# Performance work log

Measured on AMD Instinct MI355X. Metric: run time of the kernel, lower is better.

Reference implementation:

```python
import jax, jax.numpy as jnp
import numpy as np

B, T, C = 4, 4096, 1024
H = 16
D = C // H
EPS = 1e-06


def setup_inputs() -> dict:
    key = jax.random.key(0)
    k1, k2, k3 = jax.random.split(key, 3)
    x = jax.random.normal(k1, (B, T, C), dtype=jnp.float32)
    Wqkv = jax.random.normal(k2, (3 * C, C), dtype=jnp.float32) * (1.0 / np.sqrt(C))
    Wproj = jax.random.normal(k3, (C, C), dtype=jnp.float32) * (1.0 / np.sqrt(C))
    bproj = jnp.zeros((C,), dtype=jnp.float32)
    return {"x": x, "Wqkv": Wqkv, "Wproj": Wproj, "bproj": bproj}


def _phi(x):
    # elu(x) + 1 kernel feature map (non-negative)
    return jax.nn.elu(x) + 1.0


def reference(x, Wqkv, Wproj, bproj):
    b, t, c = x.shape
    qkv = jnp.einsum('btc,ec->bte', x, Wqkv)              # (B,T,3C)
    qkv = qkv.reshape(b, t, 3, H, D)
    q, k, v = qkv[:, :, 0], qkv[:, :, 1], qkv[:, :, 2]     # (B,T,H,D)
    q = _phi(q)
    k = _phi(k)
    # kv state: sum over sequence of outer products k_d v_m -> (B,H,D,D)
    kv = jnp.einsum('bnhd,bnhm->bhdm', k, v)
    k_sum = k.sum(axis=1)                                  # (B,H,D)
    out = jnp.einsum('bnhd,bhdm->bnhm', q, kv)             # (B,T,H,D)
    normalizer = jnp.einsum('bnhd,bhd->bnh', q, k_sum) + EPS
    out = out / normalizer[..., None]
    out = out.reshape(b, t, c)
    out = jnp.einsum('btc,oc->bto', out, Wproj) + bproj
    return out
```

## Files before the change

### kernel.cpp

```cpp
#include <hip/hip_runtime.h>

typedef __bf16 bf16;
typedef bf16 bf16x8 __attribute__((ext_vector_type(8)));
typedef bf16 bf16x4 __attribute__((ext_vector_type(4)));
typedef float f32x4 __attribute__((ext_vector_type(4)));

#define B_ 4
#define T_ 4096
#define C_ 1024
#define EPS_ 1e-6f
#define KVTSTR 16448

typedef __attribute__((address_space(1))) const void* as1p;
typedef __attribute__((address_space(3))) void* as3p;

__global__ void cast_kernel(const float* __restrict__ in, bf16* __restrict__ out, int n8) {
  int i = blockIdx.x * blockDim.x + threadIdx.x;
  int stride = gridDim.x * blockDim.x;
  for (; i < n8; i += stride) {
    const float4* p = (const float4*)(in + (size_t)i * 8);
    float4 v0 = p[0];
    float4 v1 = p[1];
    bf16x8 o;
    o[0] = (bf16)v0.x; o[1] = (bf16)v0.y; o[2] = (bf16)v0.z; o[3] = (bf16)v0.w;
    o[4] = (bf16)v1.x; o[5] = (bf16)v1.y; o[6] = (bf16)v1.z; o[7] = (bf16)v1.w;
    *(bf16x8*)(out + (size_t)i * 8) = o;
  }
}

#define BM 256
#define BN 128
#define BK 32
#define KD 1024
#define NT (KD / BK)
#define ABYT (BM * BK * 2)
#define BUFB ((BM + BN) * BK * 2)
#define SMEMB (6 * BUFB)

#define GSTEP(CURA, CURB, NXTA, NXTB, T)                                                   \
  do {                                                                                     \
    const bool pf = (T) + 5 < NT;                                                          \
    if (pf) {                                                                              \
      const int ko = ((T) + 5) * BK;                                                       \
      __builtin_amdgcn_global_load_lds((as1p)(pA0 + ko), (as3p)(smem + sb + tid * 16), 16, 0, 0);          \
      __builtin_amdgcn_global_load_lds((as1p)(pA1 + ko), (as3p)(smem + sb + 8192 + tid * 16), 16, 0, 0);   \
      __builtin_amdgcn_global_load_lds((as1p)(pB0 + ko), (as3p)(smem + sb + 16384 + tid * 16), 16, 0, 0);  \
    }                                                                                      \
    {                                                                                      \
      const bf16* Ab = (const bf16*)(smem + rb);                                           \
      const bf16* Bb = (const bf16*)(smem + rb + ABYT);                                    \
      _Pragma("unroll") for (int mi = 0; mi < 4; mi++)                                     \
          NXTA[mi] = *(const bf16x8*)(Ab + (wm * 64 + mi * 16 + fr) * 32 + fsw);           \
      _Pragma("unroll") for (int nj = 0; nj < 4; nj++)                                     \
          NXTB[nj] = *(const bf16x8*)(Bb + (wn * 64 + nj * 16 + fr) * 32 + fsw);           \
    }                                                                                      \
    __builtin_amdgcn_s_setprio(1);                                                         \
    _Pragma("unroll") for (int mi = 0; mi < 4; mi++)                                       \
        _Pragma("unroll") for (int nj = 0; nj < 4; nj++)                                   \
            acc[mi][nj] = __builtin_amdgcn_mfma_f32_16x16x32_bf16(CURA[mi], CURB[nj], acc[mi][nj], 0, 0, 0); \
    __builtin_amdgcn_s_setprio(0);                                                         \
    asm volatile("s_waitcnt lgkmcnt(0)" ::: "memory");                                     \
    if (pf) asm volatile("s_waitcnt vmcnt(9)" ::: "memory");                               \
    else    asm volatile("s_waitcnt vmcnt(0)" ::: "memory");                               \
    __builtin_amdgcn_s_barrier();                                                          \
    __builtin_amdgcn_sched_barrier(0);                                                     \
    rb += BUFB; if (rb >= SMEMB) rb -= SMEMB;                                              \
    sb += BUFB; if (sb >= SMEMB) sb -= SMEMB;                                              \
  } while (0)

template <int MODE>
__global__ __launch_bounds__(512, 1) void gemm5(
    const bf16* __restrict__ A, const bf16* __restrict__ Bm,
    void* __restrict__ Cout, const float* __restrict__ bias,
    bf16* __restrict__ kvt, int M, int N, int tiles_n) {
  extern __shared__ char smem[];
  const int tid = threadIdx.x;
  const int l = tid & 63;
  const int w = tid >> 6;
  const int wm = w >> 1;
  const int wn = w & 1;

  const int cpx = gridDim.x >> 3;
  const int bid = (blockIdx.x & 7) * cpx + (blockIdx.x >> 3);
  const int tm = (bid / tiles_n) * BM;
  const int tn = (bid % tiles_n) * BN;

  const int srow = tid >> 2;
  const int g8 = ((tid & 3) ^ ((tid >> 3) & 3)) * 8;

  const bf16* pA0 = A + (size_t)(tm + srow) * KD + g8;
  const bf16* pA1 = A + (size_t)(tm + 128 + srow) * KD + g8;
  const bf16* pB0 = Bm + (size_t)(tn + srow) * KD + g8;

  const int fr = l & 15;
  const int fc = l >> 4;
  const int fsw = (fc ^ ((fr >> 1) & 3)) * 8;

  f32x4 acc[4][4] = {};
  bf16x8 afA[4], bfA[4], afB[4], bfB[4];

#pragma unroll
  for (int kt = 0; kt < 5; kt++) {
    __builtin_amdgcn_global_load_lds((as1p)(pA0 + kt * BK), (as3p)(smem + kt * BUFB + tid * 16), 16, 0, 0);
    __builtin_amdgcn_global_load_lds((as1p)(pA1 + kt * BK), (as3p)(smem + kt * BUFB + 8192 + tid * 16), 16, 0, 0);
    __builtin_amdgcn_global_load_lds((as1p)(pB0 + kt * BK), (as3p)(smem + kt * BUFB + 16384 + tid * 16), 16, 0, 0);
  }
  asm volatile("s_waitcnt vmcnt(9)" ::: "memory");
  __builtin_amdgcn_s_barrier();
  __builtin_amdgcn_sched_barrier(0);

  {
    const bf16* Ab = (const bf16*)(smem);
    const bf16* Bb = (const bf16*)(smem + ABYT);
#pragma unroll
    for (int mi = 0; mi < 4; mi++)
      afA[mi] = *(const bf16x8*)(Ab + (wm * 64 + mi * 16 + fr) * 32 + fsw);
#pragma unroll
    for (int nj = 0; nj < 4; nj++)
      bfA[nj] = *(const bf16x8*)(Bb + (wn * 64 + nj * 16 + fr) * 32 + fsw);
  }

  int rb = BUFB;
  int sb = 5 * BUFB;
  for (int t = 0; t < NT; t += 2) {
    GSTEP(afA, bfA, afB, bfB, t);
    GSTEP(afB, bfB, afA, bfA, t + 1);
  }

  const int crow0 = tm + wm * 64 + (l >> 4) * 4;
  const int ccol0 = tn + wn * 64 + (l & 15);
  if (MODE == 0) {
    if (tn < 1024) {
      bf16* qbuf = (bf16*)Cout;
#pragma unroll
      for (int mi = 0; mi < 4; mi++)
#pragma unroll
        for (int nj = 0; nj < 4; nj++) {
          const int col = ccol0 + nj * 16;
#pragma unroll
          for (int r = 0; r < 4; r++) {
            const int row = crow0 + mi * 16 + r;
            float v = acc[mi][nj][r];
            v = (v > 0.f) ? (v + 1.0f) : __expf(v);
            qbuf[(size_t)row * 1024 + col] = (bf16)v;
          }
        }
    } else {
#pragma unroll
      for (int mi = 0; mi < 4; mi++)
#pragma unroll
        for (int nj = 0; nj < 4; nj++) {
          const int colp = ccol0 + nj * 16 - 1024;
          const bool isk = (colp < 1024);
          bf16x4 pk;
#pragma unroll
          for (int r = 0; r < 4; r++) {
            float v = acc[mi][nj][r];
            if (isk) v = (v > 0.f) ? (v + 1.0f) : __expf(v);
            pk[r] = (bf16)v;
          }
          const int n0 = crow0 + mi * 16;
          *(bf16x4*)(kvt + (size_t)colp * KVTSTR + n0) = pk;
        }
    }
  } else {
    float* Cf = (float*)Cout;
#pragma unroll
    for (int mi = 0; mi < 4; mi++)
#pragma unroll
      for (int nj = 0; nj < 4; nj++) {
        const int col = ccol0 + nj * 16;
        const float bv = bias[col];
#pragma unroll
        for (int r = 0; r < 4; r++) {
          const int row = crow0 + mi * 16 + r;
          Cf[(size_t)row * N + col] = acc[mi][nj][r] + bv;
        }
      }
  }
}

__global__ __launch_bounds__(256) void kvgemm(const bf16* __restrict__ kvt,
                                              float* __restrict__ partial) {
  const int kc = blockIdx.x >> 6;
  const int bh = blockIdx.x & 63;
  const int b = bh >> 4, h = bh & 15;
  const int l = threadIdx.x & 63;
  const int w = threadIdx.x >> 6;

  const size_t nb = (size_t)b * 4096 + kc * 1024 + (l >> 4) * 8;
  const bf16* Ar = kvt + (size_t)(h * 64 + w * 16 + (l & 15)) * KVTSTR + nb;
  const bf16* Br = kvt + (size_t)(1024 + h * 64 + (l & 15)) * KVTSTR + nb;

  f32x4 acc[4] = {};
  float ks = 0.f;
  bf16x8 aC, bC[4], aN, bN[4];
  aC = *(const bf16x8*)Ar;
#pragma unroll
  for (int nj = 0; nj < 4; nj++) bC[nj] = *(const bf16x8*)(Br + (size_t)nj * 16 * KVTSTR);

  for (int it = 0; it < 32; ++it) {
    if (it + 1 < 32) {
      aN = *(const bf16x8*)(Ar + (it + 1) * 32);
#pragma unroll
      for (int nj = 0; nj < 4; nj++)
        bN[nj] = *(const bf16x8*)(Br + (size_t)nj * 16 * KVTSTR + (it + 1) * 32);
    }
#pragma unroll
    for (int i = 0; i < 8; i++) ks += (float)aC[i];
#pragma unroll
    for (int nj = 0; nj < 4; nj++)
      acc[nj] = __builtin_amdgcn_mfma_f32_16x16x32_bf16(aC, bC[nj], acc[nj], 0, 0, 0);
    aC = aN;
#pragma unroll
    for (int nj = 0; nj < 4; nj++) bC[nj] = bN[nj];
  }

  ks += __shfl_xor(ks, 16);
  ks += __shfl_xor(ks, 32);

  float* p = partial + (size_t)(kc * 64 + bh) * 4160;
#pragma unroll
  for (int nj = 0; nj < 4; nj++) {
    const int m = nj * 16 + (l & 15);
#pragma unroll
    for (int r = 0; r < 4; r++) {
      const int d = w * 16 + (l >> 4) * 4 + r;
      p[d * 64 + m] = acc[nj][r];
    }
  }
  if (l < 16) p[4096 + w * 16 + l] = ks;
}

__global__ void kv_finalize(const float* __restrict__ partial, bf16* __restrict__ kvb) {
  const int bh = blockIdx.x;
  for (int i = threadIdx.x; i < 80 * 64; i += 256) {
    const int row = i >> 6;
    const int dd = i & 63;
    float outv = 0.f;
    if (row < 64) {
      float s = 0.f;
#pragma unroll
      for (int kc = 0; kc < 4; kc++)
        s += partial[(size_t)(kc * 64 + bh) * 4160 + dd * 64 + row];
      outv = s;
    } else if (row < 66) {
      float s = 0.f;
#pragma unroll
      for (int kc = 0; kc < 4; kc++)
        s += partial[(size_t)(kc * 64 + bh) * 4160 + 4096 + dd];
      bf16 hi = (bf16)s;
      outv = (row == 64) ? (float)hi : (s - (float)hi);
    }
    kvb[(size_t)bh * 5120 + row * 64 + dd] = (bf16)outv;
  }
}

__global__ __launch_bounds__(256) void attn_mfma(const bf16* __restrict__ qbuf,
                                                 const bf16* __restrict__ kvb,
                                                 bf16* __restrict__ attn) {
  const int bh = blockIdx.x >> 4;
  const int tch = blockIdx.x & 15;
  const int b = bh >> 4;
  const int h = bh & 15;
  const int lane = threadIdx.x & 63;
  const int wave = threadIdx.x >> 6;
  const int t0 = tch * 256 + wave * 64;

  const bf16* kvp = kvb + (size_t)bh * 5120;
  bf16x8 bfrag[5][2];
#pragma unroll
  for (int j = 0; j < 5; j++)
#pragma unroll
    for (int kk = 0; kk < 2; kk++)
      bfrag[j][kk] = *(const bf16x8*)(kvp + (j * 16 + (lane & 15)) * 64 + kk * 32 + (lane >> 4) * 8);

  f32x4 acc[4][5] = {};
#pragma unroll
  for (int i = 0; i < 4; i++) {
    const int t = t0 + i * 16 + (lane & 15);
    const bf16* qp = qbuf + (size_t)(b * T_ + t) * 1024 + h * 64 + (lane >> 4) * 8;
    bf16x8 a0 = *(const bf16x8*)qp;
    bf16x8 a1 = *(const bf16x8*)(qp + 32);
#pragma unroll
    for (int j = 0; j < 5; j++) {
      acc[i][j] = __builtin_amdgcn_mfma_f32_16x16x32_bf16(a0, bfrag[j][0], acc[i][j], 0, 0, 0);
      acc[i][j] = __builtin_amdgcn_mfma_f32_16x16x32_bf16(a1, bfrag[j][1], acc[i][j], 0, 0, 0);
    }
  }

#pragma unroll
  for (int i = 0; i < 4; i++) {
#pragma unroll
    for (int r = 0; r < 4; r++) {
      float hi = __shfl(acc[i][4][r], (lane & 48));
      float lo = __shfl(acc[i][4][r], (lane & 48) + 1);
      float inv = 1.0f / (hi + lo + EPS_);
      const int t = t0 + i * 16 + (lane >> 4) * 4 + r;
      bf16* op = attn + (size_t)(b * T_ + t) * 1024 + h * 64 + (lane & 15);
#pragma unroll
      for (int j = 0; j < 4; j++)
        op[j * 16] = (bf16)(acc[i][j][r] * inv);
    }
  }
}

extern "C" void kernel_launch(void* const* d_in, const int* in_sizes, int n_in,
                              void* d_out, int out_size, void* d_ws, size_t ws_size,
                              hipStream_t stream) {
  const float* x = (const float*)d_in[0];
  const float* Wqkv = (const float*)d_in[1];
  const float* Wproj = (const float*)d_in[2];
  const float* bproj = (const float*)d_in[3];
  float* out = (float*)d_out;

  char* w = (char*)d_ws;
  bf16* xw = (bf16*)w;      w += (size_t)16777216 * 2;
  bf16* wqkv = (bf16*)w;    w += (size_t)3145728 * 2;
  bf16* wproj = (bf16*)w;   w += (size_t)1048576 * 2;
  bf16* qbuf = (bf16*)w;    w += (size_t)16384 * 1024 * 2;
  bf16* kvt = (bf16*)w;     w += (size_t)2048 * KVTSTR * 2;
  bf16* attnb = (bf16*)w;   w += (size_t)16384 * 1024 * 2;
  float* partial = (float*)w; w += (size_t)4 * 64 * 4160 * 4;
  bf16* kvb = (bf16*)w;

  (void)hipFuncSetAttribute((const void*)gemm5<0>,
      hipFuncAttributeMaxDynamicSharedMemorySize, SMEMB);
  (void)hipFuncSetAttribute((const void*)gemm5<1>,
      hipFuncAttributeMaxDynamicSharedMemorySize, SMEMB);

  cast_kernel<<<8192, 256, 0, stream>>>(x, xw, 16777216 / 8);
  cast_kernel<<<1536, 256, 0, stream>>>(Wqkv, wqkv, 3145728 / 8);
  cast_kernel<<<512, 256, 0, stream>>>(Wproj, wproj, 1048576 / 8);

  gemm5<0><<<1536, 512, SMEMB, stream>>>(xw, wqkv, (void*)qbuf, nullptr, kvt, 16384, 3072, 24);

  kvgemm<<<256, 256, 0, stream>>>(kvt, partial);
  kv_finalize<<<64, 256, 0, stream>>>(partial, kvb);

  attn_mfma<<<64 * 16, 256, 0, stream>>>(qbuf, kvb, attnb);

  gemm5<1><<<512, 512, SMEMB, stream>>>(attnb, wproj, (void*)out, bproj, nullptr, 16384, 1024, 8);
}
```

Before: 256.8 us.

## Enlarge GEMM tile to 256x256 with 4-stage LDS pipeline and 2x4 warp grid

Raises the GEMM block tile N dimension from 128 to 256, so each wave computes a 128x64 sub-tile with 8x4 MFMA accumulators. The LDS ring shrinks from 6 stages to 4 and the prefetch distance from 5 to 3, with buffer indices computed from the step number instead of rotating offsets. The aim is more arithmetic per LDS/global byte and fewer blocks. In exchange it doubles accumulator register pressure, shortens latency hiding, and leaves the output projection with only 256 blocks, which may underfill the GPU.

```diff
diff --git a/kernel.cpp b/kernel.cpp
--- a/kernel.cpp
+++ b/kernel.cpp
@@ -29,47 +29,47 @@
 }
 
 #define BM 256
-#define BN 128
+#define BN 256
 #define BK 32
 #define KD 1024
 #define NT (KD / BK)
 #define ABYT (BM * BK * 2)
-#define BUFB ((BM + BN) * BK * 2)
-#define SMEMB (6 * BUFB)
-
-#define GSTEP(CURA, CURB, NXTA, NXTB, T)                                                   \
-  do {                                                                                     \
-    const bool pf = (T) + 5 < NT;                                                          \
-    if (pf) {                                                                              \
-      const int ko = ((T) + 5) * BK;                                                       \
-      __builtin_amdgcn_global_load_lds((as1p)(pA0 + ko), (as3p)(smem + sb + tid * 16), 16, 0, 0);          \
-      __builtin_amdgcn_global_load_lds((as1p)(pA1 + ko), (as3p)(smem + sb + 8192 + tid * 16), 16, 0, 0);   \
-      __builtin_amdgcn_global_load_lds((as1p)(pB0 + ko), (as3p)(smem + sb + 16384 + tid * 16), 16, 0, 0);  \
-    }                                                                                      \
-    {                                                                                      \
-      const bf16* Ab = (const bf16*)(smem + rb);                                           \
-      const bf16* Bb = (const bf16*)(smem + rb + ABYT);                                    \
-      _Pragma("unroll") for (int mi = 0; mi < 4; mi++)                                     \
-          NXTA[mi] = *(const bf16x8*)(Ab + (wm * 64 + mi * 16 + fr) * 32 + fsw);           \
-      _Pragma("unroll") for (int nj = 0; nj < 4; nj++)                                     \
-          NXTB[nj] = *(const bf16x8*)(Bb + (wn * 64 + nj * 16 + fr) * 32 + fsw);           \
-    }                                                                                      \
-    __builtin_amdgcn_s_setprio(1);                                                         \
-    _Pragma("unroll") for (int mi = 0; mi < 4; mi++)                                       \
-        _Pragma("unroll") for (int nj = 0; nj < 4; nj++)                                   \
+#define BUFB (2 * ABYT)
+#define SMEMB (4 * BUFB)
+
+#define GSTEP(CURA, CURB, NXTA, NXTB, T)                                                       \
+  do {                                                                                         \
+    const bool st = (T) + 3 < NT;                                                              \
+    if (st) {                                                                                  \
+      const int ko = ((T) + 3) * BK;                                                           \
+      char* db = smem + (((T) + 3) & 3) * BUFB;                                                \
+      __builtin_amdgcn_global_load_lds((as1p)(pA0 + ko), (as3p)(db + tid * 16), 16, 0, 0);     \
+      __builtin_amdgcn_global_load_lds((as1p)(pA1 + ko), (as3p)(db + 8192 + tid * 16), 16, 0, 0);   \
+      __builtin_amdgcn_global_load_lds((as1p)(pB0 + ko), (as3p)(db + 16384 + tid * 16), 16, 0, 0);  \
+      __builtin_amdgcn_global_load_lds((as1p)(pB1 + ko), (as3p)(db + 24576 + tid * 16), 16, 0, 0);  \
+    }                                                                                          \
+    if ((T) + 1 < NT) {                                                                        \
+      const bf16* Ab = (const bf16*)(smem + (((T) + 1) & 3) * BUFB);                           \
+      const bf16* Bb = Ab + BM * BK;                                                           \
+      _Pragma("unroll") for (int mi = 0; mi < 8; mi++)                                         \
+          NXTA[mi] = *(const bf16x8*)(Ab + (wm * 128 + mi * 16 + fr) * 32 + fsw);              \
+      _Pragma("unroll") for (int nj = 0; nj < 4; nj++)                                         \
+          NXTB[nj] = *(const bf16x8*)(Bb + (wn * 64 + nj * 16 + fr) * 32 + fsw);               \
+    }                                                                                          \
+    __builtin_amdgcn_s_setprio(1);                                                             \
+    _Pragma("unroll") for (int mi = 0; mi < 8; mi++)                                           \
+        _Pragma("unroll") for (int nj = 0; nj < 4; nj++)                                       \
             acc[mi][nj] = __builtin_amdgcn_mfma_f32_16x16x32_bf16(CURA[mi], CURB[nj], acc[mi][nj], 0, 0, 0); \
-    __builtin_amdgcn_s_setprio(0);                                                         \
-    asm volatile("s_waitcnt lgkmcnt(0)" ::: "memory");                                     \
-    if (pf) asm volatile("s_waitcnt vmcnt(9)" ::: "memory");                               \
-    else    asm volatile("s_waitcnt vmcnt(0)" ::: "memory");                               \
-    __builtin_amdgcn_s_barrier();                                                          \
-    __builtin_amdgcn_sched_barrier(0);                                                     \
-    rb += BUFB; if (rb >= SMEMB) rb -= SMEMB;                                              \
-    sb += BUFB; if (sb >= SMEMB) sb -= SMEMB;                                              \
+    __builtin_amdgcn_s_setprio(0);                                                             \
+    asm volatile("s_waitcnt lgkmcnt(0)" ::: "memory");                                         \
+    if (st) asm volatile("s_waitcnt vmcnt(4)" ::: "memory");                                   \
+    else    asm volatile("s_waitcnt vmcnt(0)" ::: "memory");                                   \
+    __builtin_amdgcn_s_barrier();                                                              \
+    __builtin_amdgcn_sched_barrier(0);                                                         \
   } while (0)
 
 template <int MODE>
-__global__ __launch_bounds__(512, 1) void gemm5(
+__global__ __launch_bounds__(512, 1) void gemm6(
     const bf16* __restrict__ A, const bf16* __restrict__ Bm,
     void* __restrict__ Cout, const float* __restrict__ bias,
     bf16* __restrict__ kvt, int M, int N, int tiles_n) {
@@ -77,8 +77,8 @@
   const int tid = threadIdx.x;
   const int l = tid & 63;
   const int w = tid >> 6;
-  const int wm = w >> 1;
-  const int wn = w & 1;
+  const int wm = w >> 2;
+  const int wn = w & 3;
 
   const int cpx = gridDim.x >> 3;
   const int bid = (blockIdx.x & 7) * cpx + (blockIdx.x >> 3);
@@ -91,49 +91,52 @@
   const bf16* pA0 = A + (size_t)(tm + srow) * KD + g8;
   const bf16* pA1 = A + (size_t)(tm + 128 + srow) * KD + g8;
   const bf16* pB0 = Bm + (size_t)(tn + srow) * KD + g8;
+  const bf16* pB1 = Bm + (size_t)(tn + 128 + srow) * KD + g8;
 
   const int fr = l & 15;
   const int fc = l >> 4;
   const int fsw = (fc ^ ((fr >> 1) & 3)) * 8;
 
-  f32x4 acc[4][4] = {};
-  bf16x8 afA[4], bfA[4], afB[4], bfB[4];
-
-#pragma unroll
-  for (int kt = 0; kt < 5; kt++) {
-    __builtin_amdgcn_global_load_lds((as1p)(pA0 + kt * BK), (as3p)(smem + kt * BUFB + tid * 16), 16, 0, 0);
-    __builtin_amdgcn_global_load_lds((as1p)(pA1 + kt * BK), (as3p)(smem + kt * BUFB + 8192 + tid * 16), 16, 0, 0);
-    __builtin_amdgcn_global_load_lds((as1p)(pB0 + kt * BK), (as3p)(smem + kt * BUFB + 16384 + tid * 16), 16, 0, 0);
-  }
-  asm volatile("s_waitcnt vmcnt(9)" ::: "memory");
+  f32x4 acc[8][4] = {};
+  bf16x8 afA[8], bfA[4], afB[8], bfB[4];
+
+#pragma unroll
+  for (int kt = 0; kt < 3; kt++) {
+    char* db = smem + kt * BUFB;
+    __builtin_amdgcn_global_load_lds((as1p)(pA0 + kt * BK), (as3p)(db + tid * 16), 16, 0, 0);
+    __builtin_amdgcn_global_load_lds((as1p)(pA1 + kt * BK), (as3p)(db + 8192 + tid * 16), 16, 0, 0);
+    __builtin_amdgcn_global_load_lds((as1p)(pB0 + kt * BK), (as3p)(db + 16384 + tid * 16), 16, 0, 0);
+    __builtin_amdgcn_global_load_lds((as1p)(pB1 + kt * BK), (as3p)(db + 24576 + tid * 16), 16, 0, 0);
+  }
+  asm volatile("s_waitcnt vmcnt(4)" ::: "memory");
   __builtin_amdgcn_s_barrier();
   __builtin_amdgcn_sched_barrier(0);
 
   {
     const bf16* Ab = (const bf16*)(smem);
-    const bf16* Bb = (const bf16*)(smem + ABYT);
-#pragma unroll
-    for (int mi = 0; mi < 4; mi++)
-      afA[mi] = *(const bf16x8*)(Ab + (wm * 64 + mi * 16 + fr) * 32 + fsw);
+    const bf16* Bb = Ab + BM * BK;
+#pragma unroll
+    for (int mi = 0; mi < 8; mi++)
+      afA[mi] = *(const bf16x8*)(Ab + (wm * 128 + mi * 16 + fr) * 32 + fsw);
 #pragma unroll
     for (int nj = 0; nj < 4; nj++)
       bfA[nj] = *(const bf16x8*)(Bb + (wn * 64 + nj * 16 + fr) * 32 + fsw);
   }
-
-  int rb = BUFB;
-  int sb = 5 * BUFB;
+  asm volatile("s_waitcnt lgkmcnt(0)" ::: "memory");
+  __builtin_amdgcn_sched_barrier(0);
+
   for (int t = 0; t < NT; t += 2) {
     GSTEP(afA, bfA, afB, bfB, t);
     GSTEP(afB, bfB, afA, bfA, t + 1);
   }
 
-  const int crow0 = tm + wm * 64 + (l >> 4) * 4;
+  const int crow0 = tm + wm * 128 + (l >> 4) * 4;
   const int ccol0 = tn + wn * 64 + (l & 15);
   if (MODE == 0) {
     if (tn < 1024) {
       bf16* qbuf = (bf16*)Cout;
 #pragma unroll
-      for (int mi = 0; mi < 4; mi++)
+      for (int mi = 0; mi < 8; mi++)
 #pragma unroll
         for (int nj = 0; nj < 4; nj++) {
           const int col = ccol0 + nj * 16;
@@ -147,7 +150,7 @@
         }
     } else {
 #pragma unroll
-      for (int mi = 0; mi < 4; mi++)
+      for (int mi = 0; mi < 8; mi++)
 #pragma unroll
         for (int nj = 0; nj < 4; nj++) {
           const int colp = ccol0 + nj * 16 - 1024;
@@ -166,7 +169,7 @@
   } else {
     float* Cf = (float*)Cout;
 #pragma unroll
-    for (int mi = 0; mi < 4; mi++)
+    for (int mi = 0; mi < 8; mi++)
 #pragma unroll
       for (int nj = 0; nj < 4; nj++) {
         const int col = ccol0 + nj * 16;
@@ -324,21 +327,21 @@
   float* partial = (float*)w; w += (size_t)4 * 64 * 4160 * 4;
   bf16* kvb = (bf16*)w;
 
-  (void)hipFuncSetAttribute((const void*)gemm5<0>,
+  (void)hipFuncSetAttribute((const void*)gemm6<0>,
       hipFuncAttributeMaxDynamicSharedMemorySize, SMEMB);
-  (void)hipFuncSetAttribute((const void*)gemm5<1>,
+  (void)hipFuncSetAttribute((const void*)gemm6<1>,
       hipFuncAttributeMaxDynamicSharedMemorySize, SMEMB);
 
   cast_kernel<<<8192, 256, 0, stream>>>(x, xw, 16777216 / 8);
   cast_kernel<<<1536, 256, 0, stream>>>(Wqkv, wqkv, 3145728 / 8);
   cast_kernel<<<512, 256, 0, stream>>>(Wproj, wproj, 1048576 / 8);
 
-  gemm5<0><<<1536, 512, SMEMB, stream>>>(xw, wqkv, (void*)qbuf, nullptr, kvt, 16384, 3072, 24);
+  gemm6<0><<<768, 512, SMEMB, stream>>>(xw, wqkv, (void*)qbuf, nullptr, kvt, 16384, 3072, 12);
 
   kvgemm<<<256, 256, 0, stream>>>(kvt, partial);
   kv_finalize<<<64, 256, 0, stream>>>(partial, kvb);
 
   attn_mfma<<<64 * 16, 256, 0, stream>>>(qbuf, kvb, attnb);
 
-  gemm5<1><<<512, 512, SMEMB, stream>>>(attnb, wproj, (void*)out, bproj, nullptr, 16384, 1024, 8);
-}
+  gemm6<1><<<256, 512, SMEMB, stream>>>(attnb, wproj, (void*)out, bproj, nullptr, 16384, 1024, 4);
+}
```

Result: faster. 228.3 us (-11.1%).
